# Optimization experiments

Measured on AMD Instinct MI355X. Metric: run time of the kernel, lower is better.

Reference implementation:

```python
import jax, jax.numpy as jnp
import numpy as np

NEG_SLOPE = 0.2

def gat_conv(x, edge_index, W, a_src, a_dst, b):
    # PyG GATConv, heads=1, eval mode (dropout off), add_self_loops=True
    N = x.shape[0]
    h = x @ W                                   # [N, C]
    loops = jnp.arange(N, dtype=edge_index.dtype)
    src = jnp.concatenate([edge_index[0], loops])
    dst = jnp.concatenate([edge_index[1], loops])
    s_src = h @ a_src                            # [N]
    s_dst = h @ a_dst                            # [N]
    e = s_src[src] + s_dst[dst]                  # [E+N]
    e = jnp.where(e > 0, e, NEG_SLOPE * e)       # leaky_relu
    # segment softmax over destination neighborhoods
    m = jax.ops.segment_max(e, dst, num_segments=N)
    ex = jnp.exp(e - m[dst])
    denom = jax.ops.segment_sum(ex, dst, num_segments=N)
    alpha = ex / denom[dst]                      # [E+N]
    out = jax.ops.segment_sum(alpha[:, None] * h[src], dst, num_segments=N)
    return out + b

def setup_inputs() -> dict:
    key = jax.random.key(0)
    ks = jax.random.split(key, 10)
    N, F_in, H, C, E = 100000, 256, 128, 40, 1600000
    x = jax.random.normal(ks[0], (N, F_in), dtype=jnp.float32)
    edge_index = jax.random.randint(ks[1], (2, E), 0, N, dtype=jnp.int64)
    s1 = 1.0 / np.sqrt(F_in)
    s2 = 1.0 / np.sqrt(H)
    W1 = jax.random.normal(ks[2], (F_in, H), dtype=jnp.float32) * s1
    a_src1 = jax.random.normal(ks[3], (H,), dtype=jnp.float32) * s2
    a_dst1 = jax.random.normal(ks[4], (H,), dtype=jnp.float32) * s2
    b1 = jnp.zeros((H,), dtype=jnp.float32)
    W2 = jax.random.normal(ks[5], (H, C), dtype=jnp.float32) * s2
    a_src2 = jax.random.normal(ks[6], (C,), dtype=jnp.float32) * 0.1
    a_dst2 = jax.random.normal(ks[7], (C,), dtype=jnp.float32) * 0.1
    b2 = jnp.zeros((C,), dtype=jnp.float32)
    return {"x": x, "edge_index": edge_index, "W1": W1, "a_src1": a_src1,
            "a_dst1": a_dst1, "b1": b1, "W2": W2, "a_src2": a_src2,
            "a_dst2": a_dst2, "b2": b2}

def reference(x, edge_index, W1, a_src1, a_dst1, b1, W2, a_src2, a_dst2, b2):
    h = gat_conv(x, edge_index, W1, a_src1, a_dst1, b1)
    h = jax.nn.relu(h)
    # dropout(p=0.6) is identity in eval mode
    h = gat_conv(h, edge_index, W2, a_src2, a_dst2, b2)
    return jax.nn.log_softmax(h, axis=1)
```

## Files before the change

kernel.cpp:

```cpp
#include <hip/hip_runtime.h>
#include <math.h>

#define NEG_SLOPE 0.2f
#define CAP 64
#define NB 64
#define NBUCKET 1563
#define BCAP 1408
#define CHUNK 8192
#define NBINBLK 196

typedef __attribute__((ext_vector_type(8))) short short8;
typedef __attribute__((ext_vector_type(4))) short short4v;
typedef __attribute__((ext_vector_type(4))) float f32x4;
typedef __attribute__((ext_vector_type(2))) float f32x2;

__device__ inline unsigned short f2bf(float f) {
    union { float f; unsigned u; } x; x.f = f;
    unsigned r = x.u + 0x7FFFu + ((x.u >> 16) & 1u);
    return (unsigned short)(r >> 16);
}

__device__ __forceinline__ void gload_lds16(const void* g, void* l) {
    __builtin_amdgcn_global_load_lds(
        (const __attribute__((address_space(1))) void*)g,
        (__attribute__((address_space(3))) void*)l, 16, 0, 0);
}


__global__ __launch_bounds__(256) void front_kernel(
    const int* __restrict__ ei, int* __restrict__ bcnt,
    unsigned* __restrict__ bbuf, int E,
    const float* __restrict__ W1, const float* __restrict__ W2,
    short* __restrict__ bsw1, short* __restrict__ bsw2)
{
    __shared__ int lc[NBUCKET];
    __shared__ int lsrc[CHUNK];
    __shared__ int ldst[CHUNK];
    const int tid = threadIdx.x;

    if (blockIdx.x < NBINBLK) {
        const int base = blockIdx.x * CHUNK;
        const int n = (E - base < CHUNK) ? (E - base) : CHUNK;

        for (int b = tid; b < NBUCKET; b += 256) lc[b] = 0;
        __syncthreads();

        for (int i = tid; i < n; i += 256) {
            int s = ei[base + i];
            int d = ei[E + base + i];
            lsrc[i] = s;
            ldst[i] = d;
            atomicAdd(&lc[d >> 6], 1);
        }
        __syncthreads();

        for (int b = tid; b < NBUCKET; b += 256) {
            int c = lc[b];
            lc[b] = c ? atomicAdd(&bcnt[b], c) : 0;
        }
        __syncthreads();

        for (int i = tid; i < n; i += 256) {
            int s = lsrc[i];
            int d = ldst[i];
            int b = d >> 6;
            int pos = atomicAdd(&lc[b], 1);
            if (pos < BCAP)
                bbuf[(size_t)b * BCAP + pos] = (unsigned)s | ((unsigned)(d & 63) << 17);
        }
    } else {
        int t = (blockIdx.x - NBINBLK) * 256 + tid;
        if (t < 4096) {
            int lane = t & 63;
            int f = t >> 6;
            int k_step = f & 7;
            int n_tile = f >> 3;
            int n  = n_tile * 16 + (lane & 15);
            int k0 = k_step * 32 + (lane >> 4) * 8;
            short8 v;
            #pragma unroll
            for (int j = 0; j < 8; j++)
                v[j] = (short)f2bf(W1[(size_t)(k0 + j) * 128 + n]);
            ((short8*)bsw1)[t] = v;
        } else if (t < 4096 + 768) {
            int u = t - 4096;
            int lane = u & 63;
            int f = u >> 6;
            int k_step = f & 3;
            int n_tile = f >> 2;
            int n  = n_tile * 16 + (lane & 15);
            int k0 = k_step * 32 + (lane >> 4) * 8;
            short8 v;
            #pragma unroll
            for (int j = 0; j < 8; j++)
                v[j] = (n < 40) ? (short)f2bf(W2[(size_t)(k0 + j) * 40 + n]) : (short)0;
            ((short8*)bsw2)[u] = v;
        }
    }
}

__global__ __launch_bounds__(256) void mid_kernel(
    const int* __restrict__ bcnt, const unsigned* __restrict__ bbuf,
    int* __restrict__ csr, int* __restrict__ sorted, int* __restrict__ clsCnt,
    const float* __restrict__ x, const short* __restrict__ bsw,
    const float* __restrict__ a_src, const float* __restrict__ a_dst,
    unsigned char* __restrict__ h1, float* __restrict__ s_src,
    float* __restrict__ s_dst, int M)
{
    __shared__ __align__(16) char smem[16896];
    const int tid = threadIdx.x;

    if (blockIdx.x < NBUCKET) {
        int* lcnt = (int*)smem;
        int (*lcsr)[CAP] = (int(*)[CAP])(smem + 256);
        int* chist = (int*)(smem + 256 + 16384);
        int* cbase = (int*)(smem + 256 + 16384 + 16);

        const int b = blockIdx.x;
        const int nb = b * NB;

        if (tid < NB) lcnt[tid] = 0;
        if (tid < 4) chist[tid] = 0;
        __syncthreads();

        if (tid < NB && nb + tid < M) {
            int pos = atomicAdd(&lcnt[tid], 1);
            if (pos < CAP) lcsr[tid][pos] = nb + tid;
        }

        int ne = bcnt[b]; if (ne > BCAP) ne = BCAP;
        const unsigned* __restrict__ bp = bbuf + (size_t)b * BCAP;
        for (int j = tid; j < ne; j += 256) {
            unsigned v = bp[j];
            int s  = v & 0x1FFFF;
            int dl = v >> 17;
            int pos = atomicAdd(&lcnt[dl], 1);
            if (pos < CAP) lcsr[dl][pos] = s;
        }
        __syncthreads();

        const int4* __restrict__ srcp = (const int4*)&lcsr[0][0];
        int4* __restrict__ dstp = (int4*)(csr + (size_t)nb * CAP);
        #pragma unroll 4
        for (int j = tid; j < NB * CAP / 4; j += 256) dstp[j] = srcp[j];

        int deg = 0, cls = 0, pos = 0;
        bool isNode = (tid < NB && nb + tid < M);
        if (isNode) {
            deg = lcnt[tid]; if (deg > CAP) deg = CAP;
            cls = (deg - 1) >> 4;
            pos = atomicAdd(&chist[cls], 1);
        }
        __syncthreads();
        if (tid < 4) cbase[tid] = chist[tid] ? atomicAdd(&clsCnt[tid], chist[tid]) : 0;
        __syncthreads();
        if (isNode)
            sorted[(size_t)cls * M + cbase[cls] + pos] = (nb + tid) | (deg << 17);
        return;
    }

    const int wave = tid >> 6, lane = tid & 63;
    short8* lbs = (short8*)smem;
    const int rowBase = (blockIdx.x - NBUCKET) * 64;
    const int arow = rowBase + wave * 16 + (lane & 15);
    const int acol0 = (lane >> 4) * 8;
    const bool rv = (arow < M);
    const float* __restrict__ xr = x + (size_t)arow * 256 + acol0;
    const char* __restrict__ bsb = (const char*)bsw;

    auto stage = [&](int buf, int nt) {
        const char* s = bsb + nt * 8192 + wave * 2048 + lane * 16;
        char* d = smem + buf * 8192 + wave * 2048 + lane * 16;
        gload_lds16(s, d);
        gload_lds16(s + 1024, d + 1024);
    };

    stage(0, 0);

    short8 a[8];
    #pragma unroll
    for (int k = 0; k < 8; k++) {
        float4 p = make_float4(0.f, 0.f, 0.f, 0.f);
        float4 q = p;
        if (rv) {
            p = *(const float4*)(xr + k * 32);
            q = *(const float4*)(xr + k * 32 + 4);
        }
        short8 t;
        t[0] = (short)f2bf(p.x); t[1] = (short)f2bf(p.y);
        t[2] = (short)f2bf(p.z); t[3] = (short)f2bf(p.w);
        t[4] = (short)f2bf(q.x); t[5] = (short)f2bf(q.y);
        t[6] = (short)f2bf(q.z); t[7] = (short)f2bf(q.w);
        a[k] = t;
    }

    const int R0 = rowBase + wave * 16 + (lane >> 4) * 4;
    const int Cb = lane & 15;

    float asv[8], adv[8];
    #pragma unroll
    for (int nt = 0; nt < 8; nt++) {
        asv[nt] = a_src[nt * 16 + Cb];
        adv[nt] = a_dst[nt * 16 + Cb];
    }

    stage(1, 1);

    float ss[4] = {0.f, 0.f, 0.f, 0.f};
    float sd[4] = {0.f, 0.f, 0.f, 0.f};
    f32x4 prev = {0.f, 0.f, 0.f, 0.f};
    int wpk[4][4];

    #pragma unroll
    for (int nt = 0; nt < 8; nt++) {
        if (nt == 7) asm volatile("s_waitcnt vmcnt(0)" ::: "memory");
        else         asm volatile("s_waitcnt vmcnt(2)" ::: "memory");
        __builtin_amdgcn_s_barrier();

        short8 breg[8];
        #pragma unroll
        for (int k = 0; k < 8; k++) breg[k] = lbs[(nt & 1) * 512 + k * 64 + lane];
        asm volatile("s_waitcnt lgkmcnt(0)" ::: "memory");
        __builtin_amdgcn_sched_barrier(0);
        __builtin_amdgcn_s_barrier();

        if (nt < 6) stage(nt & 1, nt + 2);

        f32x4 acc = {0.f, 0.f, 0.f, 0.f};
        #pragma unroll
        for (int k = 0; k < 8; k++)
            acc = __builtin_amdgcn_mfma_f32_16x16x32_bf16(a[k], breg[k], acc, 0, 0, 0);

        float as_ = asv[nt], ad_ = adv[nt];
        #pragma unroll
        for (int r = 0; r < 4; r++) {
            float v = acc[r];
            ss[r] = fmaf(v, as_, ss[r]);
            sd[r] = fmaf(v, ad_, sd[r]);
        }
        if (nt & 1) {
            #pragma unroll
            for (int r = 0; r < 4; r++)
                wpk[nt >> 1][r] = __builtin_amdgcn_cvt_pk_fp8_f32(prev[r], acc[r], 0, false);
        } else {
            prev = acc;
        }
    }

    #pragma unroll
    for (int r = 0; r < 4; r++) {
        int R = R0 + r;
        if (R < M) {
            #pragma unroll
            for (int t = 0; t < 4; t++)
                *(unsigned short*)(h1 + (size_t)R * 128 + t * 32 + 2 * Cb) =
                    (unsigned short)wpk[t][r];
        }
    }
    #pragma unroll
    for (int off = 1; off < 16; off <<= 1) {
        #pragma unroll
        for (int r = 0; r < 4; r++) {
            ss[r] += __shfl_xor(ss[r], off);
            sd[r] += __shfl_xor(sd[r], off);
        }
    }
    if ((lane & 15) == 0) {
        #pragma unroll
        for (int r = 0; r < 4; r++) {
            int R = R0 + r;
            if (R < M) { s_src[R] = ss[r]; s_dst[R] = sd[r]; }
        }
    }
}

__global__ __launch_bounds__(256) void gemm2_kernel(
    const unsigned short* __restrict__ out1, const short* __restrict__ bsw,
    const float* __restrict__ a_src, const float* __restrict__ a_dst,
    unsigned char* __restrict__ h2, float* __restrict__ s_src,
    float* __restrict__ s_dst, int M)
{
    __shared__ __align__(16) char smem[12288];
    const int tid = threadIdx.x;
    const int wave = tid >> 6, lane = tid & 63;

    {
        const char* s = (const char*)bsw;
        #pragma unroll
        for (int c = 0; c < 3; c++) {
            int o = (wave + c * 4) * 1024 + lane * 16;
            gload_lds16(s + o, smem + o);
        }
    }

    const int rowBase = blockIdx.x * 64;
    const int arow = rowBase + wave * 16 + (lane & 15);
    const int acol0 = (lane >> 4) * 8;
    const bool rv = (arow < M);
    const unsigned short* __restrict__ orow = out1 + (size_t)arow * 128 + acol0;

    short8 a[4];
    #pragma unroll
    for (int k = 0; k < 4; k++) {
        short8 v = {0, 0, 0, 0, 0, 0, 0, 0};
        if (rv) v = *(const short8*)(orow + k * 32);
        a[k] = v;
    }

    asm volatile("s_waitcnt vmcnt(0)" ::: "memory");
    __syncthreads();

    const short8* lbs = (const short8*)smem;
    const int R0 = rowBase + wave * 16 + (lane >> 4) * 4;
    const int Cb = lane & 15;

    float accs[3][4];
    float ss[4] = {0.f, 0.f, 0.f, 0.f};
    float sd[4] = {0.f, 0.f, 0.f, 0.f};

    #pragma unroll
    for (int nt = 0; nt < 3; nt++) {
        f32x4 acc = {0.f, 0.f, 0.f, 0.f};
        #pragma unroll
        for (int k = 0; k < 4; k++) {
            short8 b = lbs[(nt * 4 + k) * 64 + lane];
            acc = __builtin_amdgcn_mfma_f32_16x16x32_bf16(a[k], b, acc, 0, 0, 0);
        }
        int C = nt * 16 + Cb;
        bool valid = (C < 40);
        float as_ = valid ? a_src[C] : 0.f;
        float ad_ = valid ? a_dst[C] : 0.f;
        #pragma unroll
        for (int r = 0; r < 4; r++) {
            float v = acc[r];
            accs[nt][r] = v;
            ss[r] = fmaf(v, as_, ss[r]);
            sd[r] = fmaf(v, ad_, sd[r]);
        }
    }
    #pragma unroll
    for (int r = 0; r < 4; r++) {
        int R = R0 + r;
        if (R < M) {
            int wA = __builtin_amdgcn_cvt_pk_fp8_f32(accs[0][r], accs[1][r], 0, false);
            int wB = __builtin_amdgcn_cvt_pk_fp8_f32(accs[2][r], 0.f, 0, false);
            *(unsigned short*)(h2 + (size_t)R * 64 + 2 * Cb) = (unsigned short)wA;
            *(unsigned short*)(h2 + (size_t)R * 64 + 32 + 2 * Cb) = (unsigned short)wB;
        }
    }
    #pragma unroll
    for (int off = 1; off < 16; off <<= 1) {
        #pragma unroll
        for (int r = 0; r < 4; r++) {
            ss[r] += __shfl_xor(ss[r], off);
            sd[r] += __shfl_xor(sd[r], off);
        }
    }
    if ((lane & 15) == 0) {
        #pragma unroll
        for (int r = 0; r < 4; r++) {
            int R = R0 + r;
            if (R < M) { s_src[R] = ss[r]; s_dst[R] = sd[r]; }
        }
    }
}

__global__ __launch_bounds__(256) void agg1_kernel(
    const unsigned char* __restrict__ h, const int* __restrict__ csr,
    const int* __restrict__ sorted, const int* __restrict__ clsCnt,
    const float* __restrict__ s_src, const float* __restrict__ s_dst,
    const float* __restrict__ bias, unsigned short* __restrict__ out1, int N)
{
    const int lane = threadIdx.x & 63;
    const int c = lane & 15;
    const int base = lane & 48;
    const int g = blockIdx.x * 16 + (threadIdx.x >> 4);
    const int cls = blockIdx.x / (100000 / 16);
    const int local = g - cls * 100000;
    if (local >= clsCnt[cls]) return;
    int ent = sorted[(size_t)cls * N + local];
    int n = ent & 0x1FFFF;
    int deg = ent >> 17;
    const int* __restrict__ edges = csr + (size_t)n * CAP;
    float sdn = s_dst[n];

    int s0 = 0, s1 = 0, s2 = 0, s3 = 0;
    float e0 = -1e30f, e1 = -1e30f, e2 = -1e30f, e3 = -1e30f;
    if (c < deg)      { s0 = edges[c];      e0 = s_src[s0] + sdn; }
    if (c + 16 < deg) { s1 = edges[c + 16]; e1 = s_src[s1] + sdn; }
    if (c + 32 < deg) { s2 = edges[c + 32]; e2 = s_src[s2] + sdn; }
    if (c + 48 < deg) { s3 = edges[c + 48]; e3 = s_src[s3] + sdn; }
    e0 = e0 > 0.f ? e0 : NEG_SLOPE * e0;
    e1 = e1 > 0.f ? e1 : NEG_SLOPE * e1;
    e2 = e2 > 0.f ? e2 : NEG_SLOPE * e2;
    e3 = e3 > 0.f ? e3 : NEG_SLOPE * e3;
    float m = fmaxf(fmaxf(e0, e1), fmaxf(e2, e3));
    #pragma unroll
    for (int off = 1; off < 16; off <<= 1) m = fmaxf(m, __shfl_xor(m, off));
    float w0 = (c < deg)      ? __expf(e0 - m) : 0.f;
    float w1 = (c + 16 < deg) ? __expf(e1 - m) : 0.f;
    float w2 = (c + 32 < deg) ? __expf(e2 - m) : 0.f;
    float w3 = (c + 48 < deg) ? __expf(e3 - m) : 0.f;
    float denom = (w0 + w1) + (w2 + w3);
    #pragma unroll
    for (int off = 1; off < 16; off <<= 1) denom += __shfl_xor(denom, off);
    float inv = 1.0f / denom;

    const uint2* __restrict__ hp = (const uint2*)h;
    f32x2 acc0 = {0.f, 0.f}, acc1 = {0.f, 0.f}, acc2 = {0.f, 0.f}, acc3 = {0.f, 0.f};

#define AGG1_BLK(K, SK, WK)                                                  \
    if (16 * K < deg) {                                                      \
        _Pragma("unroll")                                                    \
        for (int jj = 0; jj < 16; jj++) {                                    \
            int   sv = __shfl(SK, base + jj);                                \
            float wv = __shfl(WK, base + jj);                                \
            if (16 * K + jj < deg) {                                         \
                uint2 u = hp[(size_t)sv * 16 + c];                           \
                f32x2 p;                                                     \
                p = __builtin_amdgcn_cvt_pk_f32_fp8(u.x, false); acc0 += p * wv; \
                p = __builtin_amdgcn_cvt_pk_f32_fp8(u.x, true);  acc1 += p * wv; \
                p = __builtin_amdgcn_cvt_pk_f32_fp8(u.y, false); acc2 += p * wv; \
                p = __builtin_amdgcn_cvt_pk_f32_fp8(u.y, true);  acc3 += p * wv; \
            }                                                                \
        }                                                                    \
    }
    AGG1_BLK(0, s0, w0)
    AGG1_BLK(1, s1, w1)
    AGG1_BLK(2, s2, w2)
    AGG1_BLK(3, s3, w3)
#undef AGG1_BLK

    int cA = 32 * (c >> 2) + 4 * (c & 3);
    float4 bA = *(const float4*)&bias[cA];
    float4 bB = *(const float4*)&bias[cA + 16];
    float r0 = fmaxf(fmaf(acc0.x, inv, bA.x), 0.f);
    float r1 = fmaxf(fmaf(acc1.x, inv, bA.y), 0.f);
    float r2 = fmaxf(fmaf(acc2.x, inv, bA.z), 0.f);
    float r3 = fmaxf(fmaf(acc3.x, inv, bA.w), 0.f);
    float q0 = fmaxf(fmaf(acc0.y, inv, bB.x), 0.f);
    float q1 = fmaxf(fmaf(acc1.y, inv, bB.y), 0.f);
    float q2 = fmaxf(fmaf(acc2.y, inv, bB.z), 0.f);
    float q3 = fmaxf(fmaf(acc3.y, inv, bB.w), 0.f);
    short4v oA = { (short)f2bf(r0), (short)f2bf(r1), (short)f2bf(r2), (short)f2bf(r3) };
    short4v oB = { (short)f2bf(q0), (short)f2bf(q1), (short)f2bf(q2), (short)f2bf(q3) };
    *(short4v*)&out1[(size_t)n * 128 + cA] = oA;
    *(short4v*)&out1[(size_t)n * 128 + cA + 16] = oB;
}

__global__ __launch_bounds__(256) void agg2_kernel(
    const unsigned char* __restrict__ h, const int* __restrict__ csr,
    const int* __restrict__ sorted, const int* __restrict__ clsCnt,
    const float* __restrict__ s_src, const float* __restrict__ s_dst,
    const float* __restrict__ bias, float* __restrict__ out, int N)
{
    const int lane = threadIdx.x & 63;
    const int c = lane & 15;
    const int base = lane & 48;
    const int g = blockIdx.x * 16 + (threadIdx.x >> 4);
    const int cls = blockIdx.x / (100000 / 16);
    const int local = g - cls * 100000;
    if (local >= clsCnt[cls]) return;
    int ent = sorted[(size_t)cls * N + local];
    int n = ent & 0x1FFFF;
    int deg = ent >> 17;
    const int* __restrict__ edges = csr + (size_t)n * CAP;
    float sdn = s_dst[n];

    int s0 = 0, s1 = 0, s2 = 0, s3 = 0;
    float e0 = -1e30f, e1 = -1e30f, e2 = -1e30f, e3 = -1e30f;
    if (c < deg)      { s0 = edges[c];      e0 = s_src[s0] + sdn; }
    if (c + 16 < deg) { s1 = edges[c + 16]; e1 = s_src[s1] + sdn; }
    if (c + 32 < deg) { s2 = edges[c + 32]; e2 = s_src[s2] + sdn; }
    if (c + 48 < deg) { s3 = edges[c + 48]; e3 = s_src[s3] + sdn; }
    e0 = e0 > 0.f ? e0 : NEG_SLOPE * e0;
    e1 = e1 > 0.f ? e1 : NEG_SLOPE * e1;
    e2 = e2 > 0.f ? e2 : NEG_SLOPE * e2;
    e3 = e3 > 0.f ? e3 : NEG_SLOPE * e3;
    float m = fmaxf(fmaxf(e0, e1), fmaxf(e2, e3));
    #pragma unroll
    for (int off = 1; off < 16; off <<= 1) m = fmaxf(m, __shfl_xor(m, off));
    float w0 = (c < deg)      ? __expf(e0 - m) : 0.f;
    float w1 = (c + 16 < deg) ? __expf(e1 - m) : 0.f;
    float w2 = (c + 32 < deg) ? __expf(e2 - m) : 0.f;
    float w3 = (c + 48 < deg) ? __expf(e3 - m) : 0.f;
    float denom = (w0 + w1) + (w2 + w3);
    #pragma unroll
    for (int off = 1; off < 16; off <<= 1) denom += __shfl_xor(denom, off);
    float inv = 1.0f / denom;

    const unsigned* __restrict__ hp = (const unsigned*)h;
    f32x2 acc0 = {0.f, 0.f}, acc1 = {0.f, 0.f};

#define AGG2_BLK(K, SK, WK)                                                  \
    if (16 * K < deg) {                                                      \
        _Pragma("unroll")                                                    \
        for (int jj = 0; jj < 16; jj++) {                                    \
            int   sv = __shfl(SK, base + jj);                                \
            float wv = __shfl(WK, base + jj);                                \
            if (16 * K + jj < deg) {                                         \
                unsigned u = hp[(size_t)sv * 16 + c];                        \
                f32x2 p;                                                     \
                p = __builtin_amdgcn_cvt_pk_f32_fp8(u, false); acc0 += p * wv; \
                p = __builtin_amdgcn_cvt_pk_f32_fp8(u, true);  acc1 += p * wv; \
            }                                                                \
        }                                                                    \
    }
    AGG2_BLK(0, s0, w0)
    AGG2_BLK(1, s1, w1)
    AGG2_BLK(2, s2, w2)
    AGG2_BLK(3, s3, w3)
#undef AGG2_BLK

    float v0 = -1e30f, v1 = -1e30f, v2 = -1e30f, v3 = -1e30f;
    bool has01 = (c < 8), has0 = (c < 12);
    if (has01) {
        v0 = fmaf(acc0.x, inv, bias[2*c]);
        v1 = fmaf(acc0.y, inv, bias[2*c + 16]);
        v2 = fmaf(acc1.x, inv, bias[2*c + 1]);
        v3 = fmaf(acc1.y, inv, bias[2*c + 17]);
    } else if (has0) {
        v0 = fmaf(acc0.x, inv, bias[2*c + 16]);
        v2 = fmaf(acc1.x, inv, bias[2*c + 17]);
    }

    float mx = fmaxf(fmaxf(v0, v1), fmaxf(v2, v3));
    #pragma unroll
    for (int off = 1; off < 16; off <<= 1) mx = fmaxf(mx, __shfl_xor(mx, off));
    float sum = 0.f;
    if (has01) sum = __expf(v0 - mx) + __expf(v1 - mx) + __expf(v2 - mx) + __expf(v3 - mx);
    else if (has0) sum = __expf(v0 - mx) + __expf(v2 - mx);
    #pragma unroll
    for (int off = 1; off < 16; off <<= 1) sum += __shfl_xor(sum, off);
    float lg = mx + __logf(sum);

    if (has01) {
        *(float2*)&out[(size_t)n * 40 + 2*c]      = make_float2(v0 - lg, v2 - lg);
        *(float2*)&out[(size_t)n * 40 + 2*c + 16] = make_float2(v1 - lg, v3 - lg);
    } else if (has0) {
        *(float2*)&out[(size_t)n * 40 + 2*c + 16] = make_float2(v0 - lg, v2 - lg);
    }
}

extern "C" void kernel_launch(void* const* d_in, const int* in_sizes, int n_in,
                              void* d_out, int out_size, void* d_ws, size_t ws_size,
                              hipStream_t stream)
{
    const float* x      = (const float*)d_in[0];
    const int*   ei     = (const int*)d_in[1];
    const float* W1     = (const float*)d_in[2];
    const float* a_src1 = (const float*)d_in[3];
    const float* a_dst1 = (const float*)d_in[4];
    const float* b1     = (const float*)d_in[5];
    const float* W2     = (const float*)d_in[6];
    const float* a_src2 = (const float*)d_in[7];
    const float* a_dst2 = (const float*)d_in[8];
    const float* b2     = (const float*)d_in[9];
    float* out = (float*)d_out;

    const int N = 100000;
    const int E = 1600000;

    char* ws = (char*)d_ws;
    size_t off = 0;
    auto alloc = [&](size_t bytes) -> void* {
        void* p = ws + off;
        off += (bytes + 255) & ~(size_t)255;
        return p;
    };
    unsigned char*  h1b  = (unsigned char*)alloc((size_t)N * 128);
    unsigned short* out1 = (unsigned short*)alloc((size_t)N * 128 * 2);
    unsigned char*  h2b  = (unsigned char*)alloc((size_t)N * 64);
    int*   csr    = (int*)alloc((size_t)NBUCKET * NB * CAP * 4);
    int*   sorted = (int*)alloc((size_t)4 * N * 4);
    float* ss1  = (float*)alloc((size_t)N * 4);
    float* sd1  = (float*)alloc((size_t)N * 4);
    float* ss2  = (float*)alloc((size_t)N * 4);
    float* sd2  = (float*)alloc((size_t)N * 4);
    short* bsw1 = (short*)alloc((size_t)4096 * 8 * 2);
    short* bsw2 = (short*)alloc((size_t)768 * 8 * 2);
    int*   bcnt = (int*)alloc((size_t)(NBUCKET + 4) * 4);
    int*   clsCnt = bcnt + NBUCKET;
    unsigned* bbuf = (unsigned*)alloc((size_t)NBUCKET * BCAP * 4);

    hipMemsetAsync(bcnt, 0, (size_t)(NBUCKET + 4) * 4, stream);

    front_kernel<<<dim3(NBINBLK + 19), dim3(256), 0, stream>>>(
        ei, bcnt, bbuf, E, W1, W2, bsw1, bsw2);

    mid_kernel<<<dim3(NBUCKET + (N + 63) / 64), dim3(256), 0, stream>>>(
        bcnt, bbuf, csr, sorted, clsCnt,
        x, bsw1, a_src1, a_dst1, h1b, ss1, sd1, N);

    agg1_kernel<<<dim3(4 * N / 16), dim3(256), 0, stream>>>(
        h1b, csr, sorted, clsCnt, ss1, sd1, b1, out1, N);

    gemm2_kernel<<<dim3((N + 63) / 64), dim3(256), 0, stream>>>(
        out1, bsw2, a_src2, a_dst2, h2b, ss2, sd2, N);

    agg2_kernel<<<dim3(4 * N / 16), dim3(256), 0, stream>>>(
        h2b, csr, sorted, clsCnt, ss2, sd2, b2, out, N);
}
```

Before: 346.3 us.

## Fuse layer-2 GEMM into layer-1 aggregation and compact class grid indexing

Folds the second-layer projection (MFMA GEMM plus attention score dot products) into the tail of the first aggregation kernel. Each block stages its 16 aggregated rows in LDS, and one wave runs the GEMM and scatters h2 and the scores by node id. This removes the out1 round-trip through global memory and one kernel launch. Both aggregation kernels now map blocks to degree classes through prefix sums of the class counts, so the grid shrinks from 4N/16 to N/16 blocks and the empty blocks that used to exit early are gone. In exchange, three of the four waves sit idle during the GEMM phase, a block barrier is added, and the bsw2 B fragments are read from global memory instead of LDS.

```diff
diff --git a/kernel.cpp b/kernel.cpp
--- a/kernel.cpp
+++ b/kernel.cpp
@@ -274,110 +274,32 @@
     }
 }
 
-__global__ __launch_bounds__(256) void gemm2_kernel(
-    const unsigned short* __restrict__ out1, const short* __restrict__ bsw,
-    const float* __restrict__ a_src, const float* __restrict__ a_dst,
-    unsigned char* __restrict__ h2, float* __restrict__ s_src,
-    float* __restrict__ s_dst, int M)
-{
-    __shared__ __align__(16) char smem[12288];
-    const int tid = threadIdx.x;
-    const int wave = tid >> 6, lane = tid & 63;
-
-    {
-        const char* s = (const char*)bsw;
-        #pragma unroll
-        for (int c = 0; c < 3; c++) {
-            int o = (wave + c * 4) * 1024 + lane * 16;
-            gload_lds16(s + o, smem + o);
-        }
-    }
-
-    const int rowBase = blockIdx.x * 64;
-    const int arow = rowBase + wave * 16 + (lane & 15);
-    const int acol0 = (lane >> 4) * 8;
-    const bool rv = (arow < M);
-    const unsigned short* __restrict__ orow = out1 + (size_t)arow * 128 + acol0;
-
-    short8 a[4];
-    #pragma unroll
-    for (int k = 0; k < 4; k++) {
-        short8 v = {0, 0, 0, 0, 0, 0, 0, 0};
-        if (rv) v = *(const short8*)(orow + k * 32);
-        a[k] = v;
-    }
-
-    asm volatile("s_waitcnt vmcnt(0)" ::: "memory");
-    __syncthreads();
-
-    const short8* lbs = (const short8*)smem;
-    const int R0 = rowBase + wave * 16 + (lane >> 4) * 4;
-    const int Cb = lane & 15;
-
-    float accs[3][4];
-    float ss[4] = {0.f, 0.f, 0.f, 0.f};
-    float sd[4] = {0.f, 0.f, 0.f, 0.f};
-
-    #pragma unroll
-    for (int nt = 0; nt < 3; nt++) {
-        f32x4 acc = {0.f, 0.f, 0.f, 0.f};
-        #pragma unroll
-        for (int k = 0; k < 4; k++) {
-            short8 b = lbs[(nt * 4 + k) * 64 + lane];
-            acc = __builtin_amdgcn_mfma_f32_16x16x32_bf16(a[k], b, acc, 0, 0, 0);
-        }
-        int C = nt * 16 + Cb;
-        bool valid = (C < 40);
-        float as_ = valid ? a_src[C] : 0.f;
-        float ad_ = valid ? a_dst[C] : 0.f;
-        #pragma unroll
-        for (int r = 0; r < 4; r++) {
-            float v = acc[r];
-            accs[nt][r] = v;
-            ss[r] = fmaf(v, as_, ss[r]);
-            sd[r] = fmaf(v, ad_, sd[r]);
-        }
-    }
-    #pragma unroll
-    for (int r = 0; r < 4; r++) {
-        int R = R0 + r;
-        if (R < M) {
-            int wA = __builtin_amdgcn_cvt_pk_fp8_f32(accs[0][r], accs[1][r], 0, false);
-            int wB = __builtin_amdgcn_cvt_pk_fp8_f32(accs[2][r], 0.f, 0, false);
-            *(unsigned short*)(h2 + (size_t)R * 64 + 2 * Cb) = (unsigned short)wA;
-            *(unsigned short*)(h2 + (size_t)R * 64 + 32 + 2 * Cb) = (unsigned short)wB;
-        }
-    }
-    #pragma unroll
-    for (int off = 1; off < 16; off <<= 1) {
-        #pragma unroll
-        for (int r = 0; r < 4; r++) {
-            ss[r] += __shfl_xor(ss[r], off);
-            sd[r] += __shfl_xor(sd[r], off);
-        }
-    }
-    if ((lane & 15) == 0) {
-        #pragma unroll
-        for (int r = 0; r < 4; r++) {
-            int R = R0 + r;
-            if (R < M) { s_src[R] = ss[r]; s_dst[R] = sd[r]; }
-        }
-    }
-}
-
 __global__ __launch_bounds__(256) void agg1_kernel(
     const unsigned char* __restrict__ h, const int* __restrict__ csr,
     const int* __restrict__ sorted, const int* __restrict__ clsCnt,
     const float* __restrict__ s_src, const float* __restrict__ s_dst,
-    const float* __restrict__ bias, unsigned short* __restrict__ out1, int N)
+    const float* __restrict__ bias,
+    const short* __restrict__ bsw2,
+    const float* __restrict__ a_src2, const float* __restrict__ a_dst2,
+    unsigned char* __restrict__ h2, float* __restrict__ ss2,
+    float* __restrict__ sd2, int N)
 {
-    const int lane = threadIdx.x & 63;
+    __shared__ short lrow[16][136];
+    __shared__ int   lnode[16];
+    const int tid = threadIdx.x;
+    const int lane = tid & 63;
     const int c = lane & 15;
     const int base = lane & 48;
-    const int g = blockIdx.x * 16 + (threadIdx.x >> 4);
-    const int cls = blockIdx.x / (100000 / 16);
-    const int local = g - cls * 100000;
-    if (local >= clsCnt[cls]) return;
+    const int grp = tid >> 4;
+    const int g = blockIdx.x * 16 + grp;
+
+    int c0 = clsCnt[0], c01 = c0 + clsCnt[1], c012 = c01 + clsCnt[2];
+    int cls, local;
+    if (g < c0)        { cls = 0; local = g; }
+    else if (g < c01)  { cls = 1; local = g - c0; }
+    else if (g < c012) { cls = 2; local = g - c01; }
+    else               { cls = 3; local = g - c012; }
+
     int ent = sorted[(size_t)cls * N + local];
     int n = ent & 0x1FFFF;
     int deg = ent >> 17;
@@ -444,8 +366,67 @@
     float q3 = fmaxf(fmaf(acc3.y, inv, bB.w), 0.f);
     short4v oA = { (short)f2bf(r0), (short)f2bf(r1), (short)f2bf(r2), (short)f2bf(r3) };
     short4v oB = { (short)f2bf(q0), (short)f2bf(q1), (short)f2bf(q2), (short)f2bf(q3) };
-    *(short4v*)&out1[(size_t)n * 128 + cA] = oA;
-    *(short4v*)&out1[(size_t)n * 128 + cA + 16] = oB;
+    *(short4v*)&lrow[grp][cA] = oA;
+    *(short4v*)&lrow[grp][cA + 16] = oB;
+    if (c == 0) lnode[grp] = n;
+    __syncthreads();
+
+    if (tid >= 64) return;
+
+    const short8* __restrict__ bs = (const short8*)bsw2;
+    short8 a[4];
+    #pragma unroll
+    for (int k = 0; k < 4; k++)
+        a[k] = *(const short8*)&lrow[lane & 15][(lane >> 4) * 8 + k * 32];
+
+    float accs[3][4];
+    float ssv[4] = {0.f, 0.f, 0.f, 0.f};
+    float sdv[4] = {0.f, 0.f, 0.f, 0.f};
+
+    #pragma unroll
+    for (int nt = 0; nt < 3; nt++) {
+        f32x4 acc = {0.f, 0.f, 0.f, 0.f};
+        #pragma unroll
+        for (int k = 0; k < 4; k++) {
+            short8 b = bs[(nt * 4 + k) * 64 + lane];
+            acc = __builtin_amdgcn_mfma_f32_16x16x32_bf16(a[k], b, acc, 0, 0, 0);
+        }
+        int C = nt * 16 + c;
+        bool valid = (C < 40);
+        float as_ = valid ? a_src2[C] : 0.f;
+        float ad_ = valid ? a_dst2[C] : 0.f;
+        #pragma unroll
+        for (int r = 0; r < 4; r++) {
+            float v = acc[r];
+            accs[nt][r] = v;
+            ssv[r] = fmaf(v, as_, ssv[r]);
+            sdv[r] = fmaf(v, ad_, sdv[r]);
+        }
+    }
+    #pragma unroll
+    for (int r = 0; r < 4; r++) {
+        int node = lnode[(lane >> 4) * 4 + r];
+        int wA = __builtin_amdgcn_cvt_pk_fp8_f32(accs[0][r], accs[1][r], 0, false);
+        int wB = __builtin_amdgcn_cvt_pk_fp8_f32(accs[2][r], 0.f, 0, false);
+        *(unsigned short*)(h2 + (size_t)node * 64 + 2 * c) = (unsigned short)wA;
+        *(unsigned short*)(h2 + (size_t)node * 64 + 32 + 2 * c) = (unsigned short)wB;
+    }
+    #pragma unroll
+    for (int off = 1; off < 16; off <<= 1) {
+        #pragma unroll
+        for (int r = 0; r < 4; r++) {
+            ssv[r] += __shfl_xor(ssv[r], off);
+            sdv[r] += __shfl_xor(sdv[r], off);
+        }
+    }
+    if (c == 0) {
+        #pragma unroll
+        for (int r = 0; r < 4; r++) {
+            int node = lnode[(lane >> 4) * 4 + r];
+            ss2[node] = ssv[r];
+            sd2[node] = sdv[r];
+        }
+    }
 }
 
 __global__ __launch_bounds__(256) void agg2_kernel(
@@ -458,9 +439,14 @@
     const int c = lane & 15;
     const int base = lane & 48;
     const int g = blockIdx.x * 16 + (threadIdx.x >> 4);
-    const int cls = blockIdx.x / (100000 / 16);
-    const int local = g - cls * 100000;
-    if (local >= clsCnt[cls]) return;
+
+    int c0 = clsCnt[0], c01 = c0 + clsCnt[1], c012 = c01 + clsCnt[2];
+    int cls, local;
+    if (g < c0)        { cls = 0; local = g; }
+    else if (g < c01)  { cls = 1; local = g - c0; }
+    else if (g < c012) { cls = 2; local = g - c01; }
+    else               { cls = 3; local = g - c012; }
+
     int ent = sorted[(size_t)cls * N + local];
     int n = ent & 0x1FFFF;
     int deg = ent >> 17;
@@ -569,7 +555,6 @@
         return p;
     };
     unsigned char*  h1b  = (unsigned char*)alloc((size_t)N * 128);
-    unsigned short* out1 = (unsigned short*)alloc((size_t)N * 128 * 2);
     unsigned char*  h2b  = (unsigned char*)alloc((size_t)N * 64);
     int*   csr    = (int*)alloc((size_t)NBUCKET * NB * CAP * 4);
     int*   sorted = (int*)alloc((size_t)4 * N * 4);
@@ -592,12 +577,10 @@
         bcnt, bbuf, csr, sorted, clsCnt,
         x, bsw1, a_src1, a_dst1, h1b, ss1, sd1, N);
 
-    agg1_kernel<<<dim3(4 * N / 16), dim3(256), 0, stream>>>(
-        h1b, csr, sorted, clsCnt, ss1, sd1, b1, out1, N);
-
-    gemm2_kernel<<<dim3((N + 63) / 64), dim3(256), 0, stream>>>(
-        out1, bsw2, a_src2, a_dst2, h2b, ss2, sd2, N);
-
-    agg2_kernel<<<dim3(4 * N / 16), dim3(256), 0, stream>>>(
+    agg1_kernel<<<dim3(N / 16), dim3(256), 0, stream>>>(
+        h1b, csr, sorted, clsCnt, ss1, sd1, b1,
+        bsw2, a_src2, a_dst2, h2b, ss2, sd2, N);
+
+    agg2_kernel<<<dim3(N / 16), dim3(256), 0, stream>>>(
         h2b, csr, sorted, clsCnt, ss2, sd2, b2, out, N);
 }
```

Result: faster. 339.2 us (-2.0%).
